# Optimization experiments

Measured on AMD Instinct MI355X. Metric: run time of the kernel, lower is better.

Reference implementation:

```python
import jax, jax.numpy as jnp
import numpy as np

_EPS = 1e-4  # pytorch3d se3_exp_map clamps the SQUARED rotation angle at this eps


def _hat(w):
    # w: [..., 3] -> skew-symmetric [..., 3, 3]
    wx, wy, wz = w[..., 0], w[..., 1], w[..., 2]
    z = jnp.zeros_like(wx)
    return jnp.stack([
        jnp.stack([z, -wz, wy], axis=-1),
        jnp.stack([wz, z, -wx], axis=-1),
        jnp.stack([-wy, wx, z], axis=-1),
    ], axis=-2)


def _se3_exp(dofs):
    # dofs: [..., 6] = (log_translation, log_rotation), pytorch3d convention.
    # Returns R [..., 3, 3] and t [..., 3] such that p' = R @ p + t,
    # matching pytorch3d's row-convention matrix M ([:3,:3]=R^T, [3,:3]=t)
    # applied as p' = p @ M[:3,:3] + M[3,:3].
    t_log = dofs[..., :3]
    w = dofs[..., 3:]
    nrms = jnp.sum(w * w, axis=-1)
    theta = jnp.sqrt(jnp.clip(nrms, _EPS))  # [...]
    H = _hat(w)
    H2 = H @ H
    st, ct = jnp.sin(theta), jnp.cos(theta)
    f1 = (st / theta)[..., None, None]
    f2 = ((1.0 - ct) / (theta * theta))[..., None, None]
    f3 = ((theta - st) / (theta * theta * theta))[..., None, None]
    I = jnp.eye(3, dtype=dofs.dtype)
    R = I + f1 * H + f2 * H2            # Rodrigues
    V = I + f2 * H + f3 * H2            # left-Jacobian of SO(3)
    t = jnp.einsum('...ij,...j->...i', V, t_log)
    return R, t


def setup_inputs() -> dict:
    key = jax.random.key(0)
    k1, k2 = jax.random.split(key)
    B, T, N = 64, 28, 4096
    X_v = jax.random.normal(k1, (B, T, N, 3), dtype=jnp.float32)
    dofs = jax.random.normal(k2, (B, T, 6), dtype=jnp.float32)
    return {"X_v": X_v, "dofs": dofs}


def reference(X_v, dofs):
    # Fused, fully-batched version of the per-tooth python loop:
    # one SE3 exp over all (B,T) transforms + one batched point transform.
    R, t = _se3_exp(dofs)                                  # [B,T,3,3], [B,T,3]
    out = jnp.einsum('btij,btnj->btni', R, X_v) + t[:, :, None, :]
    return out
```

## Files before the change

kernel.cpp:

```cpp
#include <hip/hip_runtime.h>


__global__ __launch_bounds__(256) void se3_apply_kernel(
    const float* __restrict__ X,
    const float* __restrict__ dofs,
    float* __restrict__ out,
    int n3,
    int blocksPerBT)
{
    const int bt    = blockIdx.x / blocksPerBT;
    const int chunk = blockIdx.x - bt * blocksPerBT;

    const float* d = dofs + bt * 6;
    const float tx = d[0], ty = d[1], tz = d[2];
    const float wx = d[3], wy = d[4], wz = d[5];

    const float nrm2  = wx * wx + wy * wy + wz * wz;
    const float th2   = fmaxf(nrm2, 1e-4f);
    const float theta = sqrtf(th2);
    const float st = sinf(theta);
    const float ct = cosf(theta);
    const float f1 = st / theta;
    const float f2 = (1.0f - ct) / th2;
    const float f3 = (theta - st) / (th2 * theta);

    const float xx = wx * wx, yy = wy * wy, zz = wz * wz;
    const float xy = wx * wy, xz = wx * wz, yz = wy * wz;

    const float R00 = 1.0f - f2 * (yy + zz);
    const float R01 = f2 * xy - f1 * wz;
    const float R02 = f2 * xz + f1 * wy;
    const float R10 = f2 * xy + f1 * wz;
    const float R11 = 1.0f - f2 * (xx + zz);
    const float R12 = f2 * yz - f1 * wx;
    const float R20 = f2 * xz - f1 * wy;
    const float R21 = f2 * yz + f1 * wx;
    const float R22 = 1.0f - f2 * (xx + yy);

    const float V00 = 1.0f - f3 * (yy + zz);
    const float V01 = f3 * xy - f2 * wz;
    const float V02 = f3 * xz + f2 * wy;
    const float V10 = f3 * xy + f2 * wz;
    const float V11 = 1.0f - f3 * (xx + zz);
    const float V12 = f3 * yz - f2 * wx;
    const float V20 = f3 * xz - f2 * wy;
    const float V21 = f3 * yz + f2 * wx;
    const float V22 = 1.0f - f3 * (xx + yy);

    const float Tx = V00 * tx + V01 * ty + V02 * tz;
    const float Ty = V10 * tx + V11 * ty + V12 * tz;
    const float Tz = V20 * tx + V21 * ty + V22 * tz;

    const int tIdx = chunk * (int)blockDim.x + (int)threadIdx.x;
    const int fOff = tIdx * 12;
    if (fOff + 12 > n3) return;

    const long long base = (long long)bt * (long long)n3 + (long long)fOff;
    const float4* __restrict__ Xp = (const float4*)(X + base);
    float4* __restrict__ Op       = (float4*)(out + base);

    const float4 v0 = Xp[0];
    const float4 v1 = Xp[1];
    const float4 v2 = Xp[2];

#define SE3_TR(px, py, pz, qx, qy, qz)                                   \
    qx = fmaf(R00, px, fmaf(R01, py, fmaf(R02, pz, Tx)));                \
    qy = fmaf(R10, px, fmaf(R11, py, fmaf(R12, pz, Ty)));                \
    qz = fmaf(R20, px, fmaf(R21, py, fmaf(R22, pz, Tz)));

    float q0x, q0y, q0z, q1x, q1y, q1z, q2x, q2y, q2z, q3x, q3y, q3z;
    SE3_TR(v0.x, v0.y, v0.z, q0x, q0y, q0z);
    SE3_TR(v0.w, v1.x, v1.y, q1x, q1y, q1z);
    SE3_TR(v1.z, v1.w, v2.x, q2x, q2y, q2z);
    SE3_TR(v2.y, v2.z, v2.w, q3x, q3y, q3z);
#undef SE3_TR

    Op[0] = make_float4(q0x, q0y, q0z, q1x);
    Op[1] = make_float4(q1y, q1z, q2x, q2y);
    Op[2] = make_float4(q2z, q3x, q3y, q3z);
}

extern "C" void kernel_launch(void* const* d_in, const int* in_sizes, int n_in,
                              void* d_out, int out_size, void* d_ws, size_t ws_size,
                              hipStream_t stream) {
    const float* X    = (const float*)d_in[0];
    const float* dofs = (const float*)d_in[1];
    float* out        = (float*)d_out;

    const int BT = in_sizes[1] / 6;
    const int n3 = in_sizes[0] / BT;

    const int threadsPerBT = (n3 + 11) / 12;
    const int block = 256;
    const int blocksPerBT = (threadsPerBT + block - 1) / block;

    dim3 grid((unsigned)(BT * blocksPerBT));
    se3_apply_kernel<<<grid, block, 0, stream>>>(X, dofs, out, n3, blocksPerBT);
}
```

Before: 158.5 us.

## Stage points through LDS for fully coalesced float4 loads and stores

Each block now loads a 3072-float tile with contiguous float4 accesses across threads, stages it in shared memory, transforms points in place in LDS, then writes back coalesced float4s. Global loads are issued before the SE3 parameter computation so the two overlap. Previously each thread read three strided float4s, which leaves gaps between lanes in each access. The cost is two barriers plus LDS traffic, and the stride-3 scalar LDS accesses may hit bank conflicts.

```diff
diff --git a/kernel.cpp b/kernel.cpp
--- a/kernel.cpp
+++ b/kernel.cpp
@@ -6,10 +6,28 @@
     const float* __restrict__ dofs,
     float* __restrict__ out,
     int n3,
-    int blocksPerBT)
+    int tilesPerBT)
 {
-    const int bt    = blockIdx.x / blocksPerBT;
-    const int chunk = blockIdx.x - bt * blocksPerBT;
+    __shared__ float lds[3072];
+
+    const int bt   = blockIdx.x / tilesPerBT;
+    const int tile = blockIdx.x - bt * tilesPerBT;
+    const int t    = threadIdx.x;
+
+    const long long baseF = (long long)bt * (long long)n3 + (long long)tile * 3072;
+    const int f4InBT   = tile * 768;
+    const int n4       = n3 >> 2;
+    const float4* __restrict__ Xp = (const float4*)(X + baseF);
+    float4* __restrict__ Op       = (float4*)(out + baseF);
+    float4* lds4 = (float4*)lds;
+
+    float4 v0, v1, v2;
+    const bool g0 = (f4InBT + t        ) < n4;
+    const bool g1 = (f4InBT + t + 256  ) < n4;
+    const bool g2 = (f4InBT + t + 512  ) < n4;
+    if (g0) v0 = Xp[t];
+    if (g1) v1 = Xp[t + 256];
+    if (g2) v2 = Xp[t + 512];
 
     const float* d = dofs + bt * 6;
     const float tx = d[0], ty = d[1], tz = d[2];
@@ -51,33 +69,26 @@
     const float Ty = V10 * tx + V11 * ty + V12 * tz;
     const float Tz = V20 * tx + V21 * ty + V22 * tz;
 
-    const int tIdx = chunk * (int)blockDim.x + (int)threadIdx.x;
-    const int fOff = tIdx * 12;
-    if (fOff + 12 > n3) return;
+    if (g0) lds4[t]       = v0;
+    if (g1) lds4[t + 256] = v1;
+    if (g2) lds4[t + 512] = v2;
+    __syncthreads();
 
-    const long long base = (long long)bt * (long long)n3 + (long long)fOff;
-    const float4* __restrict__ Xp = (const float4*)(X + base);
-    float4* __restrict__ Op       = (float4*)(out + base);
+#pragma unroll
+    for (int j = 0; j < 4; ++j) {
+        const int p = 3 * (t + 256 * j);
+        const float px = lds[p + 0];
+        const float py = lds[p + 1];
+        const float pz = lds[p + 2];
+        lds[p + 0] = fmaf(R00, px, fmaf(R01, py, fmaf(R02, pz, Tx)));
+        lds[p + 1] = fmaf(R10, px, fmaf(R11, py, fmaf(R12, pz, Ty)));
+        lds[p + 2] = fmaf(R20, px, fmaf(R21, py, fmaf(R22, pz, Tz)));
+    }
+    __syncthreads();
 
-    const float4 v0 = Xp[0];
-    const float4 v1 = Xp[1];
-    const float4 v2 = Xp[2];
-
-#define SE3_TR(px, py, pz, qx, qy, qz)                                   \
-    qx = fmaf(R00, px, fmaf(R01, py, fmaf(R02, pz, Tx)));                \
-    qy = fmaf(R10, px, fmaf(R11, py, fmaf(R12, pz, Ty)));                \
-    qz = fmaf(R20, px, fmaf(R21, py, fmaf(R22, pz, Tz)));
-
-    float q0x, q0y, q0z, q1x, q1y, q1z, q2x, q2y, q2z, q3x, q3y, q3z;
-    SE3_TR(v0.x, v0.y, v0.z, q0x, q0y, q0z);
-    SE3_TR(v0.w, v1.x, v1.y, q1x, q1y, q1z);
-    SE3_TR(v1.z, v1.w, v2.x, q2x, q2y, q2z);
-    SE3_TR(v2.y, v2.z, v2.w, q3x, q3y, q3z);
-#undef SE3_TR
-
-    Op[0] = make_float4(q0x, q0y, q0z, q1x);
-    Op[1] = make_float4(q1y, q1z, q2x, q2y);
-    Op[2] = make_float4(q2z, q3x, q3y, q3z);
+    if (g0) Op[t]       = lds4[t];
+    if (g1) Op[t + 256] = lds4[t + 256];
+    if (g2) Op[t + 512] = lds4[t + 512];
 }
 
 extern "C" void kernel_launch(void* const* d_in, const int* in_sizes, int n_in,
@@ -90,10 +101,8 @@
     const int BT = in_sizes[1] / 6;
     const int n3 = in_sizes[0] / BT;
 
-    const int threadsPerBT = (n3 + 11) / 12;
-    const int block = 256;
-    const int blocksPerBT = (threadsPerBT + block - 1) / block;
+    const int tilesPerBT = (n3 + 3071) / 3072;
 
-    dim3 grid((unsigned)(BT * blocksPerBT));
-    se3_apply_kernel<<<grid, block, 0, stream>>>(X, dofs, out, n3, blocksPerBT);
+    dim3 grid((unsigned)(BT * tilesPerBT));
+    se3_apply_kernel<<<grid, 256, 0, stream>>>(X, dofs, out, n3, tilesPerBT);
 }
```

Measured after the change: 156.9 us. No clear change (-1.1%).
